# Kernel tuning notes

Hardware: AMD Instinct MI355X
Metric: run time of the kernel (lower is better)

The kernel has to match this reference:

```python
import jax, jax.numpy as jnp
import numpy as np

TOP_K = 2


def setup_inputs() -> dict:
    key = jax.random.key(0)
    k1, k2, k3, k4, k5 = jax.random.split(key, 5)
    T, H, I, E = 1024, 1024, 2816, 8
    return {
        "hidden_states": jax.random.normal(k1, (T, H), dtype=jnp.float32),
        "router_logits": jax.random.normal(k2, (T, E), dtype=jnp.float32),
        "w1": jax.random.normal(k3, (E, I, H), dtype=jnp.float32) * 0.02,
        "w3": jax.random.normal(k4, (E, I, H), dtype=jnp.float32) * 0.02,
        "w2": jax.random.normal(k5, (E, H, I), dtype=jnp.float32) * 0.02,
    }


def _gate_weights(router_logits):
    # top-k softmax with renormalization (Mixtral-style routing)
    probs = jax.nn.softmax(router_logits, axis=-1)          # [T, E]
    vals, idx = jax.lax.top_k(probs, TOP_K)                  # [T, K]
    vals = vals / jnp.sum(vals, axis=-1, keepdims=True)
    E = router_logits.shape[-1]
    # dense per-expert gate [T, E]: scatter top-k weights via one-hot
    onehot = jax.nn.one_hot(idx, E, dtype=vals.dtype)        # [T, K, E]
    return jnp.einsum("tk,tke->te", vals, onehot)


def reference(hidden_states, router_logits, w1, w3, w2):
    x = hidden_states.reshape(-1, hidden_states.shape[-1])   # [T, H]
    gate = _gate_weights(router_logits)                      # [T, E]
    # GatedMLP per expert: silu(x @ w1^T) * (x @ w3^T) @ w2^T
    h1 = jnp.einsum("th,eih->tei", x, w1)                    # [T, E, I]
    h3 = jnp.einsum("th,eih->tei", x, w3)
    act = jax.nn.silu(h1) * h3                               # [T, E, I]
    y = jnp.einsum("tei,ehi->teh", act, w2)                  # [T, E, H]
    out = jnp.einsum("teh,te->th", y, gate)                  # weighted combine
    return out
```

## Files before the change

### kernel.cpp

```cpp
#include <hip/hip_runtime.h>
#include <stdint.h>

#define T_TOK 1024
#define H_DIM 1024
#define I_DIM 2816
#define E_NUM 8

typedef __attribute__((ext_vector_type(8))) short bf16x8;
typedef __attribute__((ext_vector_type(4))) float f32x4;

struct Meta { int counts[E_NUM]; int tiles[E_NUM]; int offs[E_NUM]; };

__device__ __forceinline__ unsigned short f2b(float f) {
    unsigned u = __float_as_uint(f);
    u += 0x7fffu + ((u >> 16) & 1u);
    return (unsigned short)(u >> 16);
}

__global__ void route_kernel(const float* __restrict__ logits,
                             int* __restrict__ tok, float* __restrict__ gate,
                             Meta* __restrict__ meta) {
    __shared__ int cnt[E_NUM];
    const int tid = threadIdx.x;
    if (tid < E_NUM) cnt[tid] = 0;
    for (int j = tid; j < E_NUM * T_TOK; j += 1024) { tok[j] = 0; gate[j] = 0.f; }
    __syncthreads();

    float p[E_NUM];
    const float* lrow = logits + tid * E_NUM;
    float m = -1e30f;
    #pragma unroll
    for (int e = 0; e < E_NUM; ++e) { p[e] = lrow[e]; m = fmaxf(m, p[e]); }
    #pragma unroll
    for (int e = 0; e < E_NUM; ++e) p[e] = __expf(p[e] - m);
    int e0 = 0; float v0 = p[0];
    #pragma unroll
    for (int e = 1; e < E_NUM; ++e) if (p[e] > v0) { v0 = p[e]; e0 = e; }
    int e1 = -1; float v1 = -1.f;
    #pragma unroll
    for (int e = 0; e < E_NUM; ++e) if (e != e0 && p[e] > v1) { v1 = p[e]; e1 = e; }
    const float inv = 1.f / (v0 + v1);
    const float g0 = v0 * inv, g1 = v1 * inv;

    const int p0 = atomicAdd(&cnt[e0], 1);
    const int p1 = atomicAdd(&cnt[e1], 1);
    tok[e0 * T_TOK + p0] = tid; gate[e0 * T_TOK + p0] = g0;
    tok[e1 * T_TOK + p1] = tid; gate[e1 * T_TOK + p1] = g1;
    __syncthreads();
    if (tid == 0) {
        int off = 0;
        for (int e = 0; e < E_NUM; ++e) {
            const int c = cnt[e];
            const int t = (c + 127) >> 7;
            meta->counts[e] = c; meta->tiles[e] = t; meta->offs[e] = off;
            off += t * 128;
        }
    }
}

__global__ void cvt_x_kernel(const float* __restrict__ x, unsigned short* __restrict__ xb) {
    const int i = blockIdx.x * blockDim.x + threadIdx.x;
    const float4 v = ((const float4*)x)[i];
    ushort4 o; o.x = f2b(v.x); o.y = f2b(v.y); o.z = f2b(v.z); o.w = f2b(v.w);
    ((ushort4*)xb)[i] = o;
}

__launch_bounds__(256)
__global__ void gemm1_kernel(const unsigned short* __restrict__ xb,
                             const float* __restrict__ w1,
                             const float* __restrict__ w3,
                             const int* __restrict__ tok,
                             const Meta* __restrict__ meta,
                             unsigned short* __restrict__ act) {
    const int e = blockIdx.y;
    const int mt = blockIdx.z;
    if (mt >= meta->tiles[e]) return;
    const int it = blockIdx.x;
    const int tid = threadIdx.x;

    __shared__ __align__(16) unsigned short As[128 * 32];
    __shared__ __align__(16) unsigned short B1s[64 * 32];
    __shared__ __align__(16) unsigned short B3s[64 * 32];

    const int arow = tid >> 2, asub = tid & 3;
    const int t0 = tok[e * T_TOK + mt * 128 + arow];
    const int t1 = tok[e * T_TOK + mt * 128 + 64 + arow];
    const unsigned short* ap0 = xb + (size_t)t0 * H_DIM + asub * 8;
    const unsigned short* ap1 = xb + (size_t)t1 * H_DIM + asub * 8;
    unsigned short* al0 = &As[arow * 32 + asub * 8];
    unsigned short* al1 = &As[(64 + arow) * 32 + asub * 8];

    const int brow = tid >> 3, bsub = tid & 7;
    const size_t wbase = (size_t)e * I_DIM * H_DIM + (size_t)(it * 64) * H_DIM;
    const float* b1p0 = w1 + wbase + (size_t)brow * H_DIM + bsub * 4;
    const float* b1p1 = w1 + wbase + (size_t)(32 + brow) * H_DIM + bsub * 4;
    const float* b3p0 = w3 + wbase + (size_t)brow * H_DIM + bsub * 4;
    const float* b3p1 = w3 + wbase + (size_t)(32 + brow) * H_DIM + bsub * 4;
    unsigned short* bl10 = &B1s[brow * 32 + bsub * 4];
    unsigned short* bl11 = &B1s[(32 + brow) * 32 + bsub * 4];
    unsigned short* bl30 = &B3s[brow * 32 + bsub * 4];
    unsigned short* bl31 = &B3s[(32 + brow) * 32 + bsub * 4];

    const int wave = tid >> 6, lane = tid & 63;
    const int quad = lane >> 4, l15 = lane & 15;
    const int mbase = (wave >> 1) * 64;
    const int nbase = (wave & 1) * 32;

    f32x4 acc1[4][2], acc3[4][2];
    #pragma unroll
    for (int mi = 0; mi < 4; ++mi)
        #pragma unroll
        for (int ni = 0; ni < 2; ++ni) {
            acc1[mi][ni] = (f32x4){0.f, 0.f, 0.f, 0.f};
            acc3[mi][ni] = (f32x4){0.f, 0.f, 0.f, 0.f};
        }

    uint4 ra0 = *(const uint4*)(ap0), ra1 = *(const uint4*)(ap1);
    float4 r10 = *(const float4*)(b1p0), r11 = *(const float4*)(b1p1);
    float4 r30 = *(const float4*)(b3p0), r31 = *(const float4*)(b3p1);

    const int NK = H_DIM / 32;
    for (int ks = 0; ks < NK; ++ks) {
        __syncthreads();
        *(uint4*)al0 = ra0;
        *(uint4*)al1 = ra1;
        ushort4 c;
        c.x = f2b(r10.x); c.y = f2b(r10.y); c.z = f2b(r10.z); c.w = f2b(r10.w); *(ushort4*)bl10 = c;
        c.x = f2b(r11.x); c.y = f2b(r11.y); c.z = f2b(r11.z); c.w = f2b(r11.w); *(ushort4*)bl11 = c;
        c.x = f2b(r30.x); c.y = f2b(r30.y); c.z = f2b(r30.z); c.w = f2b(r30.w); *(ushort4*)bl30 = c;
        c.x = f2b(r31.x); c.y = f2b(r31.y); c.z = f2b(r31.z); c.w = f2b(r31.w); *(ushort4*)bl31 = c;
        __syncthreads();
        if (ks + 1 < NK) {
            const int k0 = (ks + 1) * 32;
            ra0 = *(const uint4*)(ap0 + k0);  ra1 = *(const uint4*)(ap1 + k0);
            r10 = *(const float4*)(b1p0 + k0); r11 = *(const float4*)(b1p1 + k0);
            r30 = *(const float4*)(b3p0 + k0); r31 = *(const float4*)(b3p1 + k0);
        }
        bf16x8 a[4];
        #pragma unroll
        for (int mi = 0; mi < 4; ++mi)
            a[mi] = *(const bf16x8*)&As[(mbase + mi * 16 + l15) * 32 + quad * 8];
        bf16x8 b1f[2], b3f[2];
        #pragma unroll
        for (int ni = 0; ni < 2; ++ni) {
            b1f[ni] = *(const bf16x8*)&B1s[(nbase + ni * 16 + l15) * 32 + quad * 8];
            b3f[ni] = *(const bf16x8*)&B3s[(nbase + ni * 16 + l15) * 32 + quad * 8];
        }
        #pragma unroll
        for (int mi = 0; mi < 4; ++mi)
            #pragma unroll
            for (int ni = 0; ni < 2; ++ni) {
                acc1[mi][ni] = __builtin_amdgcn_mfma_f32_16x16x32_bf16(a[mi], b1f[ni], acc1[mi][ni], 0, 0, 0);
                acc3[mi][ni] = __builtin_amdgcn_mfma_f32_16x16x32_bf16(a[mi], b3f[ni], acc3[mi][ni], 0, 0, 0);
            }
    }

    const int opad = meta->offs[e];
    #pragma unroll
    for (int mi = 0; mi < 4; ++mi)
        #pragma unroll
        for (int ni = 0; ni < 2; ++ni)
            #pragma unroll
            for (int rr = 0; rr < 4; ++rr) {
                const float v1 = acc1[mi][ni][rr];
                const float v3 = acc3[mi][ni][rr];
                const float s = v1 / (1.f + __expf(-v1)) * v3;
                const int row = opad + mt * 128 + mbase + mi * 16 + quad * 4 + rr;
                const int col = it * 64 + nbase + ni * 16 + l15;
                act[(size_t)row * I_DIM + col] = f2b(s);
            }
}

__launch_bounds__(256)
__global__ void gemm2_kernel(const unsigned short* __restrict__ act,
                             const float* __restrict__ w2,
                             const int* __restrict__ tok,
                             const float* __restrict__ gate,
                             const Meta* __restrict__ meta,
                             float* __restrict__ out) {
    const int e = blockIdx.y;
    const int mt = blockIdx.z;
    if (mt >= meta->tiles[e]) return;
    const int it = blockIdx.x;
    const int tid = threadIdx.x;
    const int opad = meta->offs[e];

    __shared__ __align__(16) unsigned short As[128 * 32];
    __shared__ __align__(16) unsigned short Bs[64 * 32];

    const int arow = tid >> 2, asub = tid & 3;
    const unsigned short* ap0 = act + (size_t)(opad + mt * 128 + arow) * I_DIM + asub * 8;
    const unsigned short* ap1 = act + (size_t)(opad + mt * 128 + 64 + arow) * I_DIM + asub * 8;
    unsigned short* al0 = &As[arow * 32 + asub * 8];
    unsigned short* al1 = &As[(64 + arow) * 32 + asub * 8];

    const int brow = tid >> 3, bsub = tid & 7;
    const size_t wbase = (size_t)e * H_DIM * I_DIM + (size_t)(it * 64) * I_DIM;
    const float* bp0 = w2 + wbase + (size_t)brow * I_DIM + bsub * 4;
    const float* bp1 = w2 + wbase + (size_t)(32 + brow) * I_DIM + bsub * 4;
    unsigned short* bl0 = &Bs[brow * 32 + bsub * 4];
    unsigned short* bl1 = &Bs[(32 + brow) * 32 + bsub * 4];

    const int wave = tid >> 6, lane = tid & 63;
    const int quad = lane >> 4, l15 = lane & 15;
    const int mbase = (wave >> 1) * 64;
    const int nbase = (wave & 1) * 32;

    f32x4 acc[4][2];
    #pragma unroll
    for (int mi = 0; mi < 4; ++mi)
        #pragma unroll
        for (int ni = 0; ni < 2; ++ni) acc[mi][ni] = (f32x4){0.f, 0.f, 0.f, 0.f};

    uint4 ra0 = *(const uint4*)(ap0), ra1 = *(const uint4*)(ap1);
    float4 rb0 = *(const float4*)(bp0), rb1 = *(const float4*)(bp1);

    const int NK = I_DIM / 32;
    for (int ks = 0; ks < NK; ++ks) {
        __syncthreads();
        *(uint4*)al0 = ra0;
        *(uint4*)al1 = ra1;
        ushort4 c;
        c.x = f2b(rb0.x); c.y = f2b(rb0.y); c.z = f2b(rb0.z); c.w = f2b(rb0.w); *(ushort4*)bl0 = c;
        c.x = f2b(rb1.x); c.y = f2b(rb1.y); c.z = f2b(rb1.z); c.w = f2b(rb1.w); *(ushort4*)bl1 = c;
        __syncthreads();
        if (ks + 1 < NK) {
            const int k0 = (ks + 1) * 32;
            ra0 = *(const uint4*)(ap0 + k0); ra1 = *(const uint4*)(ap1 + k0);
            rb0 = *(const float4*)(bp0 + k0); rb1 = *(const float4*)(bp1 + k0);
        }
        bf16x8 a[4];
        #pragma unroll
        for (int mi = 0; mi < 4; ++mi)
            a[mi] = *(const bf16x8*)&As[(mbase + mi * 16 + l15) * 32 + quad * 8];
        bf16x8 bf[2];
        #pragma unroll
        for (int ni = 0; ni < 2; ++ni)
            bf[ni] = *(const bf16x8*)&Bs[(nbase + ni * 16 + l15) * 32 + quad * 8];
        #pragma unroll
        for (int mi = 0; mi < 4; ++mi)
            #pragma unroll
            for (int ni = 0; ni < 2; ++ni)
                acc[mi][ni] = __builtin_amdgcn_mfma_f32_16x16x32_bf16(a[mi], bf[ni], acc[mi][ni], 0, 0, 0);
    }

    #pragma unroll
    for (int mi = 0; mi < 4; ++mi)
        #pragma unroll
        for (int rr = 0; rr < 4; ++rr) {
            const int r = mt * 128 + mbase + mi * 16 + quad * 4 + rr;
            const int t = tok[e * T_TOK + r];
            const float g = gate[e * T_TOK + r];
            #pragma unroll
            for (int ni = 0; ni < 2; ++ni) {
                const int col = it * 64 + nbase + ni * 16 + l15;
                atomicAdd(&out[(size_t)t * H_DIM + col], g * acc[mi][ni][rr]);
            }
        }
}

extern "C" void kernel_launch(void* const* d_in, const int* in_sizes, int n_in,
                              void* d_out, int out_size, void* d_ws, size_t ws_size,
                              hipStream_t stream) {
    const float* x      = (const float*)d_in[0];
    const float* logits = (const float*)d_in[1];
    const float* w1     = (const float*)d_in[2];
    const float* w3     = (const float*)d_in[3];
    const float* w2     = (const float*)d_in[4];
    float* out = (float*)d_out;

    char* ws = (char*)d_ws;
    int*   tok  = (int*)ws;
    float* gate = (float*)(ws + 32768);
    Meta*  meta = (Meta*)(ws + 65536);
    unsigned short* xb  = (unsigned short*)(ws + 131072);
    unsigned short* act = (unsigned short*)(ws + 131072 + 2097152);

    hipMemsetAsync(d_out, 0, (size_t)T_TOK * H_DIM * sizeof(float), stream);
    route_kernel<<<1, 1024, 0, stream>>>(logits, tok, gate, meta);
    cvt_x_kernel<<<T_TOK * H_DIM / 4 / 256, 256, 0, stream>>>(x, xb);
    gemm1_kernel<<<dim3(I_DIM / 64, E_NUM, 8), 256, 0, stream>>>(xb, w1, w3, tok, meta, act);
    gemm2_kernel<<<dim3(H_DIM / 64, E_NUM, 8), 256, 0, stream>>>(act, w2, tok, gate, meta, out);
}
```

Baseline: 392.3 us.

## Shrink M tile to 64, deepen K step, pad LDS, split-K gemm2

Cuts the token tile from 128 to 64 rows and doubles the K step per iteration to 64. LDS rows are padded to a 72-element stride to reduce bank conflicts. gemm2 is split along I into two halves that combine through the existing atomic adds, and launch bounds request 4 blocks per SM. Together these add blocks and occupancy for the small per-expert token counts, at the cost of re-reading the fp32 weights (with bf16 conversion) twice as often per token and doubling atomic traffic in gemm2.

```diff
diff --git a/kernel.cpp b/kernel.cpp
--- a/kernel.cpp
+++ b/kernel.cpp
@@ -5,6 +5,7 @@
 #define H_DIM 1024
 #define I_DIM 2816
 #define E_NUM 8
+#define LSTR 72
 
 typedef __attribute__((ext_vector_type(8))) short bf16x8;
 typedef __attribute__((ext_vector_type(4))) float f32x4;
@@ -15,6 +16,9 @@
     unsigned u = __float_as_uint(f);
     u += 0x7fffu + ((u >> 16) & 1u);
     return (unsigned short)(u >> 16);
+}
+__device__ __forceinline__ ushort4 f2b4(float4 v) {
+    ushort4 o; o.x = f2b(v.x); o.y = f2b(v.y); o.z = f2b(v.z); o.w = f2b(v.w); return o;
 }
 
 __global__ void route_kernel(const float* __restrict__ logits,
@@ -51,9 +55,9 @@
         int off = 0;
         for (int e = 0; e < E_NUM; ++e) {
             const int c = cnt[e];
-            const int t = (c + 127) >> 7;
+            const int t = (c + 63) >> 6;
             meta->counts[e] = c; meta->tiles[e] = t; meta->offs[e] = off;
-            off += t * 128;
+            off += t * 64;
         }
     }
 }
@@ -61,11 +65,10 @@
 __global__ void cvt_x_kernel(const float* __restrict__ x, unsigned short* __restrict__ xb) {
     const int i = blockIdx.x * blockDim.x + threadIdx.x;
     const float4 v = ((const float4*)x)[i];
-    ushort4 o; o.x = f2b(v.x); o.y = f2b(v.y); o.z = f2b(v.z); o.w = f2b(v.w);
-    ((ushort4*)xb)[i] = o;
-}
-
-__launch_bounds__(256)
+    ((ushort4*)xb)[i] = f2b4(v);
+}
+
+__launch_bounds__(256, 4)
 __global__ void gemm1_kernel(const unsigned short* __restrict__ xb,
                              const float* __restrict__ w1,
                              const float* __restrict__ w3,
@@ -78,86 +81,90 @@
     const int it = blockIdx.x;
     const int tid = threadIdx.x;
 
-    __shared__ __align__(16) unsigned short As[128 * 32];
-    __shared__ __align__(16) unsigned short B1s[64 * 32];
-    __shared__ __align__(16) unsigned short B3s[64 * 32];
+    __shared__ __align__(16) unsigned short As[64 * LSTR];
+    __shared__ __align__(16) unsigned short B1s[64 * LSTR];
+    __shared__ __align__(16) unsigned short B3s[64 * LSTR];
 
     const int arow = tid >> 2, asub = tid & 3;
-    const int t0 = tok[e * T_TOK + mt * 128 + arow];
-    const int t1 = tok[e * T_TOK + mt * 128 + 64 + arow];
-    const unsigned short* ap0 = xb + (size_t)t0 * H_DIM + asub * 8;
-    const unsigned short* ap1 = xb + (size_t)t1 * H_DIM + asub * 8;
-    unsigned short* al0 = &As[arow * 32 + asub * 8];
-    unsigned short* al1 = &As[(64 + arow) * 32 + asub * 8];
-
-    const int brow = tid >> 3, bsub = tid & 7;
-    const size_t wbase = (size_t)e * I_DIM * H_DIM + (size_t)(it * 64) * H_DIM;
-    const float* b1p0 = w1 + wbase + (size_t)brow * H_DIM + bsub * 4;
-    const float* b1p1 = w1 + wbase + (size_t)(32 + brow) * H_DIM + bsub * 4;
-    const float* b3p0 = w3 + wbase + (size_t)brow * H_DIM + bsub * 4;
-    const float* b3p1 = w3 + wbase + (size_t)(32 + brow) * H_DIM + bsub * 4;
-    unsigned short* bl10 = &B1s[brow * 32 + bsub * 4];
-    unsigned short* bl11 = &B1s[(32 + brow) * 32 + bsub * 4];
-    unsigned short* bl30 = &B3s[brow * 32 + bsub * 4];
-    unsigned short* bl31 = &B3s[(32 + brow) * 32 + bsub * 4];
+    const int t0 = tok[e * T_TOK + mt * 64 + arow];
+    const unsigned short* ap = xb + (size_t)t0 * H_DIM + asub * 8;
+    unsigned short* al0 = &As[arow * LSTR + asub * 8];
+    unsigned short* al1 = al0 + 32;
+
+    const size_t wb = (size_t)e * I_DIM * H_DIM + (size_t)(it * 64 + arow) * H_DIM;
+    const float* b1p = w1 + wb + asub * 4;
+    const float* b3p = w3 + wb + asub * 4;
+    unsigned short* bl1 = &B1s[arow * LSTR + asub * 4];
+    unsigned short* bl3 = &B3s[arow * LSTR + asub * 4];
 
     const int wave = tid >> 6, lane = tid & 63;
     const int quad = lane >> 4, l15 = lane & 15;
-    const int mbase = (wave >> 1) * 64;
+    const int mbase = (wave >> 1) * 32;
     const int nbase = (wave & 1) * 32;
 
-    f32x4 acc1[4][2], acc3[4][2];
-    #pragma unroll
-    for (int mi = 0; mi < 4; ++mi)
+    f32x4 acc1[2][2], acc3[2][2];
+    #pragma unroll
+    for (int mi = 0; mi < 2; ++mi)
         #pragma unroll
         for (int ni = 0; ni < 2; ++ni) {
             acc1[mi][ni] = (f32x4){0.f, 0.f, 0.f, 0.f};
             acc3[mi][ni] = (f32x4){0.f, 0.f, 0.f, 0.f};
         }
 
-    uint4 ra0 = *(const uint4*)(ap0), ra1 = *(const uint4*)(ap1);
-    float4 r10 = *(const float4*)(b1p0), r11 = *(const float4*)(b1p1);
-    float4 r30 = *(const float4*)(b3p0), r31 = *(const float4*)(b3p1);
-
-    const int NK = H_DIM / 32;
+    uint4 ra0 = *(const uint4*)(ap);
+    uint4 ra1 = *(const uint4*)(ap + 32);
+    float4 r1[4], r3[4];
+    #pragma unroll
+    for (int j = 0; j < 4; ++j) {
+        r1[j] = *(const float4*)(b1p + 16 * j);
+        r3[j] = *(const float4*)(b3p + 16 * j);
+    }
+
+    const int NK = H_DIM / 64;
     for (int ks = 0; ks < NK; ++ks) {
         __syncthreads();
         *(uint4*)al0 = ra0;
         *(uint4*)al1 = ra1;
-        ushort4 c;
-        c.x = f2b(r10.x); c.y = f2b(r10.y); c.z = f2b(r10.z); c.w = f2b(r10.w); *(ushort4*)bl10 = c;
-        c.x = f2b(r11.x); c.y = f2b(r11.y); c.z = f2b(r11.z); c.w = f2b(r11.w); *(ushort4*)bl11 = c;
-        c.x = f2b(r30.x); c.y = f2b(r30.y); c.z = f2b(r30.z); c.w = f2b(r30.w); *(ushort4*)bl30 = c;
-        c.x = f2b(r31.x); c.y = f2b(r31.y); c.z = f2b(r31.z); c.w = f2b(r31.w); *(ushort4*)bl31 = c;
+        #pragma unroll
+        for (int j = 0; j < 4; ++j) {
+            *(ushort4*)(bl1 + 16 * j) = f2b4(r1[j]);
+            *(ushort4*)(bl3 + 16 * j) = f2b4(r3[j]);
+        }
         __syncthreads();
         if (ks + 1 < NK) {
-            const int k0 = (ks + 1) * 32;
-            ra0 = *(const uint4*)(ap0 + k0);  ra1 = *(const uint4*)(ap1 + k0);
-            r10 = *(const float4*)(b1p0 + k0); r11 = *(const float4*)(b1p1 + k0);
-            r30 = *(const float4*)(b3p0 + k0); r31 = *(const float4*)(b3p1 + k0);
-        }
-        bf16x8 a[4];
-        #pragma unroll
-        for (int mi = 0; mi < 4; ++mi)
-            a[mi] = *(const bf16x8*)&As[(mbase + mi * 16 + l15) * 32 + quad * 8];
-        bf16x8 b1f[2], b3f[2];
-        #pragma unroll
-        for (int ni = 0; ni < 2; ++ni) {
-            b1f[ni] = *(const bf16x8*)&B1s[(nbase + ni * 16 + l15) * 32 + quad * 8];
-            b3f[ni] = *(const bf16x8*)&B3s[(nbase + ni * 16 + l15) * 32 + quad * 8];
-        }
-        #pragma unroll
-        for (int mi = 0; mi < 4; ++mi)
+            const int k0 = (ks + 1) * 64;
+            ra0 = *(const uint4*)(ap + k0);
+            ra1 = *(const uint4*)(ap + k0 + 32);
+            #pragma unroll
+            for (int j = 0; j < 4; ++j) {
+                r1[j] = *(const float4*)(b1p + k0 + 16 * j);
+                r3[j] = *(const float4*)(b3p + k0 + 16 * j);
+            }
+        }
+        #pragma unroll
+        for (int kk = 0; kk < 2; ++kk) {
+            bf16x8 a[2], b1f[2], b3f[2];
+            #pragma unroll
+            for (int mi = 0; mi < 2; ++mi)
+                a[mi] = *(const bf16x8*)&As[(mbase + mi * 16 + l15) * LSTR + kk * 32 + quad * 8];
             #pragma unroll
             for (int ni = 0; ni < 2; ++ni) {
-                acc1[mi][ni] = __builtin_amdgcn_mfma_f32_16x16x32_bf16(a[mi], b1f[ni], acc1[mi][ni], 0, 0, 0);
-                acc3[mi][ni] = __builtin_amdgcn_mfma_f32_16x16x32_bf16(a[mi], b3f[ni], acc3[mi][ni], 0, 0, 0);
-            }
+                b1f[ni] = *(const bf16x8*)&B1s[(nbase + ni * 16 + l15) * LSTR + kk * 32 + quad * 8];
+                b3f[ni] = *(const bf16x8*)&B3s[(nbase + ni * 16 + l15) * LSTR + kk * 32 + quad * 8];
+            }
+            #pragma unroll
+            for (int mi = 0; mi < 2; ++mi)
+                #pragma unroll
+                for (int ni = 0; ni < 2; ++ni) {
+                    acc1[mi][ni] = __builtin_amdgcn_mfma_f32_16x16x32_bf16(a[mi], b1f[ni], acc1[mi][ni], 0, 0, 0);
+                    acc3[mi][ni] = __builtin_amdgcn_mfma_f32_16x16x32_bf16(a[mi], b3f[ni], acc3[mi][ni], 0, 0, 0);
+                }
+        }
     }
 
     const int opad = meta->offs[e];
     #pragma unroll
-    for (int mi = 0; mi < 4; ++mi)
+    for (int mi = 0; mi < 2; ++mi)
         #pragma unroll
         for (int ni = 0; ni < 2; ++ni)
             #pragma unroll
@@ -165,13 +172,13 @@
                 const float v1 = acc1[mi][ni][rr];
                 const float v3 = acc3[mi][ni][rr];
                 const float s = v1 / (1.f + __expf(-v1)) * v3;
-                const int row = opad + mt * 128 + mbase + mi * 16 + quad * 4 + rr;
+                const int row = opad + mt * 64 + mbase + mi * 16 + quad * 4 + rr;
                 const int col = it * 64 + nbase + ni * 16 + l15;
                 act[(size_t)row * I_DIM + col] = f2b(s);
             }
 }
 
-__launch_bounds__(256)
+__launch_bounds__(256, 4)
 __global__ void gemm2_kernel(const unsigned short* __restrict__ act,
                              const float* __restrict__ w2,
                              const int* __restrict__ tok,
@@ -179,76 +186,80 @@
                              const Meta* __restrict__ meta,
                              float* __restrict__ out) {
     const int e = blockIdx.y;
-    const int mt = blockIdx.z;
+    const int mt = blockIdx.z >> 1;
+    const int sp = blockIdx.z & 1;
     if (mt >= meta->tiles[e]) return;
     const int it = blockIdx.x;
     const int tid = threadIdx.x;
     const int opad = meta->offs[e];
-
-    __shared__ __align__(16) unsigned short As[128 * 32];
-    __shared__ __align__(16) unsigned short Bs[64 * 32];
+    const int kbase = sp * (I_DIM / 2);
+
+    __shared__ __align__(16) unsigned short As[64 * LSTR];
+    __shared__ __align__(16) unsigned short Bs[64 * LSTR];
 
     const int arow = tid >> 2, asub = tid & 3;
-    const unsigned short* ap0 = act + (size_t)(opad + mt * 128 + arow) * I_DIM + asub * 8;
-    const unsigned short* ap1 = act + (size_t)(opad + mt * 128 + 64 + arow) * I_DIM + asub * 8;
-    unsigned short* al0 = &As[arow * 32 + asub * 8];
-    unsigned short* al1 = &As[(64 + arow) * 32 + asub * 8];
-
-    const int brow = tid >> 3, bsub = tid & 7;
-    const size_t wbase = (size_t)e * H_DIM * I_DIM + (size_t)(it * 64) * I_DIM;
-    const float* bp0 = w2 + wbase + (size_t)brow * I_DIM + bsub * 4;
-    const float* bp1 = w2 + wbase + (size_t)(32 + brow) * I_DIM + bsub * 4;
-    unsigned short* bl0 = &Bs[brow * 32 + bsub * 4];
-    unsigned short* bl1 = &Bs[(32 + brow) * 32 + bsub * 4];
+    const unsigned short* ap = act + (size_t)(opad + mt * 64 + arow) * I_DIM + kbase + asub * 8;
+    unsigned short* al0 = &As[arow * LSTR + asub * 8];
+    unsigned short* al1 = al0 + 32;
+
+    const size_t wb = (size_t)e * H_DIM * I_DIM + (size_t)(it * 64 + arow) * I_DIM + kbase;
+    const float* bp = w2 + wb + asub * 4;
+    unsigned short* bl = &Bs[arow * LSTR + asub * 4];
 
     const int wave = tid >> 6, lane = tid & 63;
     const int quad = lane >> 4, l15 = lane & 15;
-    const int mbase = (wave >> 1) * 64;
+    const int mbase = (wave >> 1) * 32;
     const int nbase = (wave & 1) * 32;
 
-    f32x4 acc[4][2];
-    #pragma unroll
-    for (int mi = 0; mi < 4; ++mi)
+    f32x4 acc[2][2];
+    #pragma unroll
+    for (int mi = 0; mi < 2; ++mi)
         #pragma unroll
         for (int ni = 0; ni < 2; ++ni) acc[mi][ni] = (f32x4){0.f, 0.f, 0.f, 0.f};
 
-    uint4 ra0 = *(const uint4*)(ap0), ra1 = *(const uint4*)(ap1);
-    float4 rb0 = *(const float4*)(bp0), rb1 = *(const float4*)(bp1);
-
-    const int NK = I_DIM / 32;
+    uint4 ra0 = *(const uint4*)(ap);
+    uint4 ra1 = *(const uint4*)(ap + 32);
+    float4 rb[4];
+    #pragma unroll
+    for (int j = 0; j < 4; ++j) rb[j] = *(const float4*)(bp + 16 * j);
+
+    const int NK = (I_DIM / 2) / 64;
     for (int ks = 0; ks < NK; ++ks) {
         __syncthreads();
         *(uint4*)al0 = ra0;
         *(uint4*)al1 = ra1;
-        ushort4 c;
-        c.x = f2b(rb0.x); c.y = f2b(rb0.y); c.z = f2b(rb0.z); c.w = f2b(rb0.w); *(ushort4*)bl0 = c;
-        c.x = f2b(rb1.x); c.y = f2b(rb1.y); c.z = f2b(rb1.z); c.w = f2b(rb1.w); *(ushort4*)bl1 = c;
+        #pragma unroll
+        for (int j = 0; j < 4; ++j) *(ushort4*)(bl + 16 * j) = f2b4(rb[j]);
         __syncthreads();
         if (ks + 1 < NK) {
-            const int k0 = (ks + 1) * 32;
-            ra0 = *(const uint4*)(ap0 + k0); ra1 = *(const uint4*)(ap1 + k0);
-            rb0 = *(const float4*)(bp0 + k0); rb1 = *(const float4*)(bp1 + k0);
-        }
-        bf16x8 a[4];
-        #pragma unroll
-        for (int mi = 0; mi < 4; ++mi)
-            a[mi] = *(const bf16x8*)&As[(mbase + mi * 16 + l15) * 32 + quad * 8];
-        bf16x8 bf[2];
-        #pragma unroll
-        for (int ni = 0; ni < 2; ++ni)
-            bf[ni] = *(const bf16x8*)&Bs[(nbase + ni * 16 + l15) * 32 + quad * 8];
-        #pragma unroll
-        for (int mi = 0; mi < 4; ++mi)
+            const int k0 = (ks + 1) * 64;
+            ra0 = *(const uint4*)(ap + k0);
+            ra1 = *(const uint4*)(ap + k0 + 32);
+            #pragma unroll
+            for (int j = 0; j < 4; ++j) rb[j] = *(const float4*)(bp + k0 + 16 * j);
+        }
+        #pragma unroll
+        for (int kk = 0; kk < 2; ++kk) {
+            bf16x8 a[2], bf[2];
+            #pragma unroll
+            for (int mi = 0; mi < 2; ++mi)
+                a[mi] = *(const bf16x8*)&As[(mbase + mi * 16 + l15) * LSTR + kk * 32 + quad * 8];
             #pragma unroll
             for (int ni = 0; ni < 2; ++ni)
-                acc[mi][ni] = __builtin_amdgcn_mfma_f32_16x16x32_bf16(a[mi], bf[ni], acc[mi][ni], 0, 0, 0);
-    }
-
-    #pragma unroll
-    for (int mi = 0; mi < 4; ++mi)
+                bf[ni] = *(const bf16x8*)&Bs[(nbase + ni * 16 + l15) * LSTR + kk * 32 + quad * 8];
+            #pragma unroll
+            for (int mi = 0; mi < 2; ++mi)
+                #pragma unroll
+                for (int ni = 0; ni < 2; ++ni)
+                    acc[mi][ni] = __builtin_amdgcn_mfma_f32_16x16x32_bf16(a[mi], bf[ni], acc[mi][ni], 0, 0, 0);
+        }
+    }
+
+    #pragma unroll
+    for (int mi = 0; mi < 2; ++mi)
         #pragma unroll
         for (int rr = 0; rr < 4; ++rr) {
-            const int r = mt * 128 + mbase + mi * 16 + quad * 4 + rr;
+            const int r = mt * 64 + mbase + mi * 16 + quad * 4 + rr;
             const int t = tok[e * T_TOK + r];
             const float g = gate[e * T_TOK + r];
             #pragma unroll
@@ -279,6 +290,6 @@
     hipMemsetAsync(d_out, 0, (size_t)T_TOK * H_DIM * sizeof(float), stream);
     route_kernel<<<1, 1024, 0, stream>>>(logits, tok, gate, meta);
     cvt_x_kernel<<<T_TOK * H_DIM / 4 / 256, 256, 0, stream>>>(x, xb);
-    gemm1_kernel<<<dim3(I_DIM / 64, E_NUM, 8), 256, 0, stream>>>(xb, w1, w3, tok, meta, act);
-    gemm2_kernel<<<dim3(H_DIM / 64, E_NUM, 8), 256, 0, stream>>>(act, w2, tok, gate, meta, out);
-}
+    gemm1_kernel<<<dim3(I_DIM / 64, E_NUM, 16), 256, 0, stream>>>(xb, w1, w3, tok, meta, act);
+    gemm2_kernel<<<dim3(H_DIM / 64, E_NUM, 32), 256, 0, stream>>>(act, w2, tok, gate, meta, out);
+}
```

After: 400.7 us. +2.2%, slower.
